# Performance work log

Hardware: AMD Instinct MI355X
Metric: run time of the kernel (lower is better)

Reference implementation:

```python
import jax, jax.numpy as jnp
import numpy as np

N, D, M, H, FF, L = 8192, 14, 36, 256, 2048, 2  # rows, d_model, material feats, mlp hidden, ffn, layers
EPS = 1e-5


def _ln(x, g, b):
    mu = jnp.mean(x, axis=-1, keepdims=True)
    var = jnp.mean((x - mu) ** 2, axis=-1, keepdims=True)
    return (x - mu) * jax.lax.rsqrt(var + EPS) * g + b


def setup_inputs() -> dict:
    key = jax.random.key(0)
    ks = iter(jax.random.split(key, 32))
    p = lambda shape, fan: jax.random.normal(next(ks), shape, jnp.float32) * (fan ** -0.5)
    return {
        "x": jax.random.normal(next(ks), (N, D), jnp.float32),
        "y": jax.random.normal(next(ks), (N, M), jnp.float32),
        # 2 post-LN TransformerEncoderLayers (nhead=1, dim_feedforward=2048, relu)
        "attn_wqkv": p((L, 3 * D, D), D), "attn_bqkv": p((L, 3 * D), D),
        "attn_wo": p((L, D, D), D), "attn_bo": p((L, D), D),
        "ln1_g": jnp.ones((L, D)), "ln1_b": jnp.zeros((L, D)),
        "ff_w1": p((L, FF, D), D), "ff_b1": p((L, FF), D),
        "ff_w2": p((L, D, FF), FF), "ff_b2": p((L, D), FF),
        "ln2_g": jnp.ones((L, D)), "ln2_b": jnp.zeros((L, D)),
        "fc1_w": p((D, D), D), "fc1_b": p((D,), D),
        "fc2_w": p((1, D), D), "fc2_b": p((1,), D),
        "fc3_w": p((H, D + M + 1), D + M + 1), "fc3_b": p((H,), D + M + 1),
        "fc4_w": p((H, H), H), "fc4_b": p((H,), H),
        "fc5_w": p((1, H), H), "fc5_b": p((1,), H),
    }


def reference(x, y, attn_wqkv, attn_bqkv, attn_wo, attn_bo, ln1_g, ln1_b,
              ff_w1, ff_b1, ff_w2, ff_b2, ln2_g, ln2_b,
              fc1_w, fc1_b, fc2_w, fc2_b, fc3_w, fc3_b, fc4_w, fc4_b, fc5_w, fc5_b):
    h = x  # [N, D]; batch of size 1 squeezed away
    for l in range(L):
        qkv = h @ attn_wqkv[l].T + attn_bqkv[l]            # [N, 3D]
        q, k, v = jnp.split(qkv, 3, axis=-1)
        scores = (q @ k.T) * (D ** -0.5)                   # [N, N]
        a = jax.nn.softmax(scores, axis=-1) @ v            # [N, D]
        a = a @ attn_wo[l].T + attn_bo[l]
        h = _ln(h + a, ln1_g[l], ln1_b[l])
        f = jax.nn.relu(h @ ff_w1[l].T + ff_b1[l]) @ ff_w2[l].T + ff_b2[l]
        h = _ln(h + f, ln2_g[l], ln2_b[l])
    x1 = h @ fc1_w.T + fc1_b                               # [N, D]
    size_out = (x1 @ fc2_w.T + fc2_b)[:, 0]                # [N]

    # batched replacement of the per-row python loop
    size_int = size_out.astype(jnp.int32)                  # trunc toward zero, like .int()
    size_f = size_int.astype(jnp.float32)[:, None]         # [N, 1]
    reg_in = jnp.concatenate([size_f, x, y], axis=1)       # [N, 1+D+M]
    r = jax.nn.relu(reg_in @ fc3_w.T + fc3_b)
    r = jax.nn.relu(r @ fc4_w.T + fc4_b)
    reg_values = (r @ fc5_w.T + fc5_b)[:, 0]               # [N]
    reg_values = jnp.where(size_int != 0, reg_values, 0.0)
    return size_out, reg_values
```

## Files before the change

kernel.cpp:

```cpp
#include <hip/hip_runtime.h>
#include <math.h>

#define NN 8192
#define DD 14
#define DP 16
#define FF 2048
#define HID 256
#define LN_EPS 1e-5f
#define QSCALE (1.4426950408889634f / 3.7416573867739413f)

typedef short bf16x8 __attribute__((ext_vector_type(8)));
typedef float f32x4 __attribute__((ext_vector_type(4)));

#define LOAD16(dst, srcp) { \
  const float4* _p = (const float4*)(srcp); \
  float4 _a = _p[0], _b = _p[1], _c = _p[2], _d = _p[3]; \
  dst[0]=_a.x; dst[1]=_a.y; dst[2]=_a.z; dst[3]=_a.w; \
  dst[4]=_b.x; dst[5]=_b.y; dst[6]=_b.z; dst[7]=_b.w; \
  dst[8]=_c.x; dst[9]=_c.y; dst[10]=_c.z; dst[11]=_c.w; \
  dst[12]=_d.x; dst[13]=_d.y; dst[14]=_d.z; dst[15]=_d.w; }

#define STORE16(dstp, src) { \
  float4* _p = (float4*)(dstp); \
  _p[0] = make_float4(src[0], src[1], src[2], src[3]); \
// ... 79 lines not shown
  VhiT[(size_t)15 * NN + r] = 0;
  VloT[(size_t)14 * NN + r] = 0;
  VloT[(size_t)15 * NN + r] = 0;
}

static __device__ __forceinline__ void store_apack(unsigned int* dst, const float* o) {
  unsigned int qp[16];
  unsigned short hh[14], ll[14];
  #pragma unroll
  for (int d = 0; d < 14; d++) {
    hh[d] = bf_hi(o[d]);
    ll[d] = bf_hi(o[d] - bf_hi_f(o[d]));
  }
  #pragma unroll
  for (int i = 0; i < 7; i++) {
    qp[i]     = (unsigned int)hh[2*i] | ((unsigned int)hh[2*i+1] << 16);
    qp[8 + i] = (unsigned int)ll[2*i] | ((unsigned int)ll[2*i+1] << 16);
  }
  qp[7] = 0; qp[15] = 0;
  uint4* d4 = (uint4*)dst;
  #pragma unroll
  for (int i = 0; i < 4; i++)
    d4[i] = make_uint4(qp[4*i], qp[4*i+1], qp[4*i+2], qp[4*i+3]);
}

static __device__ __forceinline__ void combine_ln1(
    const float* srow, const float* hr, const float* __restrict__ wo,
    const float* __restrict__ bo, const float* __restrict__ g,
    const float* __restrict__ b, float* o) {
  float L = srow[14];
  float inv = 1.f / L;
  float a[14];
  #pragma unroll
  for (int d = 0; d < 14; d++) a[d] = srow[d] * inv;
  float xx[14];
  #pragma unroll
  for (int i = 0; i < 14; i++) {
    float s = bo[i];
    #pragma unroll
    for (int d = 0; d < 14; d++) s = fmaf(wo[i * 14 + d], a[d], s);
    xx[i] = hr[i] + s;
  }
  float mu = 0.f;
  #pragma unroll
  for (int i = 0; i < 14; i++) mu += xx[i];
  mu *= (1.f / 14.f);
  float var = 0.f;
  #pragma unroll
  for (int i = 0; i < 14; i++) { float tt = xx[i] - mu; var = fmaf(tt, tt, var); }
  var *= (1.f / 14.f);
  float rs = rsqrtf(var + LN_EPS);
  #pragma unroll
  for (int i = 0; i < 14; i++) o[i] = fmaf((xx[i] - mu) * rs, g[i], b[i]);
  o[14] = 0.f; o[15] = 0.f;
}

__global__ void pack_all(const float* __restrict__ w3, const float* __restrict__ w4,
                         const float* __restrict__ ffw1, const float* __restrict__ ffw2,
                         const float* __restrict__ x, const float* __restrict__ wqkv,
                         const float* __restrict__ bqkv, float* __restrict__ h,
                         unsigned int* __restrict__ Qpack,
                         unsigned int* __restrict__ KB1, unsigned int* __restrict__ KB2,
                         unsigned short* __restrict__ VhiT, unsigned short* __restrict__ VloT,
                         unsigned short* __restrict__ B3h, unsigned short* __restrict__ B3l,
                         unsigned short* __restrict__ B4h, unsigned short* __restrict__ B4l,
                         unsigned int* __restrict__ W1B1, unsigned int* __restrict__ W1B2,
                         unsigned short* __restrict__ W2h, unsigned short* __restrict__ W2l) {
  const int blk = blockIdx.x, tid = threadIdx.x;
  if (blk < 32) {
    int t = blk * 256 + tid;
    int lane = t & 63, ks = (t >> 6) & 7, nt = t >> 9;
    int n = nt * 16 + (lane & 15);
    int k0 = ks * 32 + (lane >> 4) * 8;
    unsigned int h4[4], l4[4];
    #pragma unroll
    for (int jj = 0; jj < 4; jj++) {
      unsigned short h2[2], l2[2];
      #pragma unroll
      for (int e = 0; e < 2; e++) {
        float v = w4[(size_t)n * 256 + k0 + jj * 2 + e];
        h2[e] = bf_hi(v);
        l2[e] = bf_hi(v - bf_hi_f(v));
      }
      h4[jj] = (unsigned int)h2[0] | ((unsigned int)h2[1] << 16);
      l4[jj] = (unsigned int)l2[0] | ((unsigned int)l2[1] << 16);
    }
    ((uint4*)B4h)[t] = make_uint4(h4[0], h4[1], h4[2], h4[3]);
    ((uint4*)B4l)[t] = make_uint4(l4[0], l4[1], l4[2], l4[3]);
    if (ks < 2) {
      int fi = (nt * 2 + ks) * 64 + lane;
      #pragma unroll
      for (int jj = 0; jj < 4; jj++) {
        unsigned short h2[2], l2[2];
        #pragma unroll
        for (int e = 0; e < 2; e++) {
          int k = k0 + jj * 2 + e;
          float v = (k < 51) ? w3[(size_t)n * 51 + k] : 0.f;
          h2[e] = bf_hi(v);
          l2[e] = bf_hi(v - bf_hi_f(v));
        }
        h4[jj] = (unsigned int)h2[0] | ((unsigned int)h2[1] << 16);
        l4[jj] = (unsigned int)l2[0] | ((unsigned int)l2[1] << 16);
      }
      ((uint4*)B3h)[fi] = make_uint4(h4[0], h4[1], h4[2], h4[3]);
      ((uint4*)B3l)[fi] = make_uint4(l4[0], l4[1], l4[2], l4[3]);
    }
  } else if (blk < 48) {
    int t = (blk - 32) * 256 + tid;
    int l = t >> 11, j = t & 2047;
    const float* wrow = ffw1 + ((size_t)l * FF + j) * 14;
    unsigned int k1[16], k2[16];
    unsigned short kh[14], kl[14];
    #pragma unroll
    for (int d = 0; d < 14; d++) {
      float v = wrow[d];
      kh[d] = bf_hi(v);
      kl[d] = bf_hi(v - bf_hi_f(v));
    }
    #pragma unroll
    for (int i = 0; i < 7; i++) {
      k1[i] = (unsigned int)kh[2*i] | ((unsigned int)kh[2*i+1] << 16);
      k1[8 + i] = k1[i];
      k2[i] = (unsigned int)kl[2*i] | ((unsigned int)kl[2*i+1] << 16);
      k2[8 + i] = k2[i];
    }
    k1[7] = 0; k1[15] = 0; k2[7] = 0; k2[15] = 0;
    uint4* d1 = (uint4*)(W1B1 + (size_t)t * 16);
    uint4* d2 = (uint4*)(W1B2 + (size_t)t * 16);
    #pragma unroll
    for (int i = 0; i < 4; i++) {
      d1[i] = make_uint4(k1[4*i], k1[4*i+1], k1[4*i+2], k1[4*i+3]);
      d2[i] = make_uint4(k2[4*i], k2[4*i+1], k2[4*i+2], k2[4*i+3]);
    }
  } else if (blk < 64) {
    int t = (blk - 48) * 256 + tid;
    int l = t >> 11, j = t & 2047;
    #pragma unroll
    for (int d = 0; d < 16; d++) {
      float v = (d < 14) ? ffw2[((size_t)l * 14 + d) * FF + j] : 0.f;
      W2h[((size_t)l * 16 + d) * FF + j] = bf_hi(v);
      W2l[((size_t)l * 16 + d) * FF + j] = bf_hi(v - bf_hi_f(v));
    }
  } else {
    int r = (blk - 64) * 256 + tid;
    float hr[16];
    #pragma unroll
    for (int d = 0; d < 14; d++) hr[d] = x[(size_t)r * 14 + d];
    hr[14] = 0.f; hr[15] = 0.f;
    STORE16(h + (size_t)r * DP, hr);
    qkv_compute_store(r, hr, wqkv, bqkv, Qpack, KB1, KB2, VhiT, VloT);
  }
}

static __device__ __forceinline__ void attn_core(
    const bf16x8* __restrict__ Qp, const bf16x8* __restrict__ B1,
    const bf16x8* __restrict__ B2, const bf16x8* __restrict__ Vh,
    const bf16x8* __restrict__ Vl, int qbase, int wave, int lo4, int hi4,
    float (*Pl)[36], f32x4* o0, f32x4* o1) {
  const f32x4 zero = {0.f, 0.f, 0.f, 0.f};
  bf16x8 aQ0 = Qp[(size_t)(qbase + lo4) * 4 + hi4];
  bf16x8 aQ1 = Qp[(size_t)(qbase + 16 + lo4) * 4 + hi4];
  f32x4 acc0 = zero, acc1 = zero;
  const int kstart = wave * 1024;
  float4 ra0, ra1, rc0, rc1;
  const float4* p0 = (const float4*)&Pl[lo4][hi4 * 8];
  const float4* p1 = (const float4*)&Pl[16 + lo4][hi4 * 8];

  for (int c = 0; c < 32; c++) {
    const int kb = kstart + c * 32;
    if (c > 0) {
      ra0 = p0[0]; ra1 = p0[1]; rc0 = p1[0]; rc1 = p1[1];
      __asm__ volatile("" ::: "memory");
    }
    bf16x8 b1g0 = B1[(size_t)(kb + lo4) * 4 + hi4];
    bf16x8 b2g0 = B2[(size_t)(kb + lo4) * 4 + hi4];
    bf16x8 b1g1 = B1[(size_t)(kb + 16 + lo4) * 4 + hi4];
    bf16x8 b2g1 = B2[(size_t)(kb + 16 + lo4) * 4 + hi4];
    bf16x8 vh = Vh[(size_t)lo4 * 1024 + (kb >> 3) + hi4];
    bf16x8 vl = Vl[(size_t)lo4 * 1024 + (kb >> 3) + hi4];

    f32x4 s00 = __builtin_amdgcn_mfma_f32_16x16x32_bf16(aQ0, b1g0, zero, 0, 0, 0);
    f32x4 s01 = __builtin_amdgcn_mfma_f32_16x16x32_bf16(aQ0, b1g1, zero, 0, 0, 0);
    f32x4 s10 = __builtin_amdgcn_mfma_f32_16x16x32_bf16(aQ1, b1g0, zero, 0, 0, 0);
    f32x4 s11 = __builtin_amdgcn_mfma_f32_16x16x32_bf16(aQ1, b1g1, zero, 0, 0, 0);
    s00 = __builtin_amdgcn_mfma_f32_16x16x32_bf16(aQ0, b2g0, s00, 0, 0, 0);
    s01 = __builtin_amdgcn_mfma_f32_16x16x32_bf16(aQ0, b2g1, s01, 0, 0, 0);
    s10 = __builtin_amdgcn_mfma_f32_16x16x32_bf16(aQ1, b2g0, s10, 0, 0, 0);
    s11 = __builtin_amdgcn_mfma_f32_16x16x32_bf16(aQ1, b2g1, s11, 0, 0, 0);
    #pragma unroll
    for (int reg = 0; reg < 4; reg++) {
      Pl[hi4 * 4 + reg][lo4]           = fast_exp2(s00[reg]);
      Pl[hi4 * 4 + reg][16 + lo4]      = fast_exp2(s01[reg]);
      Pl[16 + hi4 * 4 + reg][lo4]      = fast_exp2(s10[reg]);
      Pl[16 + hi4 * 4 + reg][16 + lo4] = fast_exp2(s11[reg]);
    }
    if (c > 0) {
      const int kbp = kb - 32;
      bf16x8 vhp = Vh[(size_t)lo4 * 1024 + (kbp >> 3) + hi4];
      bf16x8 vlp = Vl[(size_t)lo4 * 1024 + (kbp >> 3) + hi4];
      float pv0[8] = {ra0.x, ra0.y, ra0.z, ra0.w, ra1.x, ra1.y, ra1.z, ra1.w};
      float pv1[8] = {rc0.x, rc0.y, rc0.z, rc0.w, rc1.x, rc1.y, rc1.z, rc1.w};
      bf16x8 ph0, pl0, ph1, pl1;
      split8(pv0, &ph0, &pl0);
      split8(pv1, &ph1, &pl1);
      acc0 = __builtin_amdgcn_mfma_f32_16x16x32_bf16(ph0, vhp, acc0, 0, 0, 0);
      acc1 = __builtin_amdgcn_mfma_f32_16x16x32_bf16(ph1, vhp, acc1, 0, 0, 0);
      acc0 = __builtin_amdgcn_mfma_f32_16x16x32_bf16(pl0, vhp, acc0, 0, 0, 0);
      acc1 = __builtin_amdgcn_mfma_f32_16x16x32_bf16(pl1, vhp, acc1, 0, 0, 0);
      acc0 = __builtin_amdgcn_mfma_f32_16x16x32_bf16(ph0, vlp, acc0, 0, 0, 0);
      acc1 = __builtin_amdgcn_mfma_f32_16x16x32_bf16(ph1, vlp, acc1, 0, 0, 0);
    }
  }
  {
    const int kbp = kstart + 31 * 32;
    bf16x8 vhp = Vh[(size_t)lo4 * 1024 + (kbp >> 3) + hi4];
    bf16x8 vlp = Vl[(size_t)lo4 * 1024 + (kbp >> 3) + hi4];
    float4 a0 = p0[0], a1 = p0[1], c0 = p1[0], c1 = p1[1];
    float pv0[8] = {a0.x, a0.y, a0.z, a0.w, a1.x, a1.y, a1.z, a1.w};
    float pv1[8] = {c0.x, c0.y, c0.z, c0.w, c1.x, c1.y, c1.z, c1.w};
    bf16x8 ph0, pl0, ph1, pl1;
    split8(pv0, &ph0, &pl0);
    split8(pv1, &ph1, &pl1);
    acc0 = __builtin_amdgcn_mfma_f32_16x16x32_bf16(ph0, vhp, acc0, 0, 0, 0);
    acc1 = __builtin_amdgcn_mfma_f32_16x16x32_bf16(ph1, vhp, acc1, 0, 0, 0);
    acc0 = __builtin_amdgcn_mfma_f32_16x16x32_bf16(pl0, vhp, acc0, 0, 0, 0);
    acc1 = __builtin_amdgcn_mfma_f32_16x16x32_bf16(pl1, vhp, acc1, 0, 0, 0);
    acc0 = __builtin_amdgcn_mfma_f32_16x16x32_bf16(ph0, vlp, acc0, 0, 0, 0);
    acc1 = __builtin_amdgcn_mfma_f32_16x16x32_bf16(ph1, vlp, acc1, 0, 0, 0);
  }
  *o0 = acc0; *o1 = acc1;
}

static __device__ __forceinline__ void ffn_core(
    bf16x8 aH0, bf16x8 aH1, const bf16x8* __restrict__ B1,
    const bf16x8* __restrict__ B2, const bf16x8* __restrict__ Vh,
    const bf16x8* __restrict__ Vl, const float* __restrict__ b1,
    int jstart, int lo4, int hi4, float (*Pl)[36], f32x4* o0, f32x4* o1) {
  const f32x4 zero = {0.f, 0.f, 0.f, 0.f};
  f32x4 acc0 = zero, acc1 = zero;
  float4 ra0, ra1, rc0, rc1;
  const float4* p0 = (const float4*)&Pl[lo4][hi4 * 8];
  const float4* p1 = (const float4*)&Pl[16 + lo4][hi4 * 8];

  for (int c = 0; c < 8; c++) {
    const int jb = jstart + c * 32;
    if (c > 0) {
      ra0 = p0[0]; ra1 = p0[1]; rc0 = p1[0]; rc1 = p1[1];
      __asm__ volatile("" ::: "memory");
    }
    bf16x8 b1g0 = B1[(size_t)(jb + lo4) * 4 + hi4];
    bf16x8 b2g0 = B2[(size_t)(jb + lo4) * 4 + hi4];
    bf16x8 b1g1 = B1[(size_t)(jb + 16 + lo4) * 4 + hi4];
    bf16x8 b2g1 = B2[(size_t)(jb + 16 + lo4) * 4 + hi4];
    float bb0 = b1[jb + lo4];
    float bb1 = b1[jb + 16 + lo4];

    f32x4 s00 = __builtin_amdgcn_mfma_f32_16x16x32_bf16(aH0, b1g0, zero, 0, 0, 0);
    f32x4 s01 = __builtin_amdgcn_mfma_f32_16x16x32_bf16(aH0, b1g1, zero, 0, 0, 0);
    f32x4 s10 = __builtin_amdgcn_mfma_f32_16x16x32_bf16(aH1, b1g0, zero, 0, 0, 0);
    f32x4 s11 = __builtin_amdgcn_mfma_f32_16x16x32_bf16(aH1, b1g1, zero, 0, 0, 0);
    s00 = __builtin_amdgcn_mfma_f32_16x16x32_bf16(aH0, b2g0, s00, 0, 0, 0);
    s01 = __builtin_amdgcn_mfma_f32_16x16x32_bf16(aH0, b2g1, s01, 0, 0, 0);
    s10 = __builtin_amdgcn_mfma_f32_16x16x32_bf16(aH1, b2g0, s10, 0, 0, 0);
    s11 = __builtin_amdgcn_mfma_f32_16x16x32_bf16(aH1, b2g1, s11, 0, 0, 0);
    #pragma unroll
    for (int reg = 0; reg < 4; reg++) {
      Pl[hi4 * 4 + reg][lo4]           = fmaxf(s00[reg] + bb0, 0.f);
      Pl[hi4 * 4 + reg][16 + lo4]      = fmaxf(s01[reg] + bb1, 0.f);
      Pl[16 + hi4 * 4 + reg][lo4]      = fmaxf(s10[reg] + bb0, 0.f);
      Pl[16 + hi4 * 4 + reg][16 + lo4] = fmaxf(s11[reg] + bb1, 0.f);
    }
    if (c > 0) {
      const int jbp = jb - 32;
      bf16x8 vhp = Vh[(size_t)lo4 * 256 + (jbp >> 3) + hi4];
      bf16x8 vlp = Vl[(size_t)lo4 * 256 + (jbp >> 3) + hi4];
      float pv0[8] = {ra0.x, ra0.y, ra0.z, ra0.w, ra1.x, ra1.y, ra1.z, ra1.w};
      float pv1[8] = {rc0.x, rc0.y, rc0.z, rc0.w, rc1.x, rc1.y, rc1.z, rc1.w};
      bf16x8 th0, tl0, th1, tl1;
      split8(pv0, &th0, &tl0);
      split8(pv1, &th1, &tl1);
      acc0 = __builtin_amdgcn_mfma_f32_16x16x32_bf16(th0, vhp, acc0, 0, 0, 0);
      acc1 = __builtin_amdgcn_mfma_f32_16x16x32_bf16(th1, vhp, acc1, 0, 0, 0);
      acc0 = __builtin_amdgcn_mfma_f32_16x16x32_bf16(tl0, vhp, acc0, 0, 0, 0);
      acc1 = __builtin_amdgcn_mfma_f32_16x16x32_bf16(tl1, vhp, acc1, 0, 0, 0);
      acc0 = __builtin_amdgcn_mfma_f32_16x16x32_bf16(th0, vlp, acc0, 0, 0, 0);
      acc1 = __builtin_amdgcn_mfma_f32_16x16x32_bf16(th1, vlp, acc1, 0, 0, 0);
    }
  }
  {
    const int jbp = jstart + 7 * 32;
    bf16x8 vhp = Vh[(size_t)lo4 * 256 + (jbp >> 3) + hi4];
    bf16x8 vlp = Vl[(size_t)lo4 * 256 + (jbp >> 3) + hi4];
    float4 a0 = p0[0], a1 = p0[1], c0 = p1[0], c1 = p1[1];
    float pv0[8] = {a0.x, a0.y, a0.z, a0.w, a1.x, a1.y, a1.z, a1.w};
    float pv1[8] = {c0.x, c0.y, c0.z, c0.w, c1.x, c1.y, c1.z, c1.w};
    bf16x8 th0, tl0, th1, tl1;
    split8(pv0, &th0, &tl0);
    split8(pv1, &th1, &tl1);
    acc0 = __builtin_amdgcn_mfma_f32_16x16x32_bf16(th0, vhp, acc0, 0, 0, 0);
    acc1 = __builtin_amdgcn_mfma_f32_16x16x32_bf16(th1, vhp, acc1, 0, 0, 0);
    acc0 = __builtin_amdgcn_mfma_f32_16x16x32_bf16(tl0, vhp, acc0, 0, 0, 0);
    acc1 = __builtin_amdgcn_mfma_f32_16x16x32_bf16(tl1, vhp, acc1, 0, 0, 0);
    acc0 = __builtin_amdgcn_mfma_f32_16x16x32_bf16(th0, vlp, acc0, 0, 0, 0);
    acc1 = __builtin_amdgcn_mfma_f32_16x16x32_bf16(th1, vlp, acc1, 0, 0, 0);
  }
  *o0 = acc0; *o1 = acc1;
}

#define SMEM_BYTES 57472

__global__ __launch_bounds__(512, 4) void layer0_fused(
    const unsigned int* __restrict__ Qpack, const unsigned int* __restrict__ KB1,
    const unsigned int* __restrict__ KB2, const unsigned short* __restrict__ VhiT,
    const unsigned short* __restrict__ VloT, float* __restrict__ h,
    const float* __restrict__ wo, const float* __restrict__ bo,
    const float* __restrict__ g1, const float* __restrict__ b1n,
    const unsigned int* __restrict__ W1B1, const unsigned int* __restrict__ W1B2,
    const unsigned short* __restrict__ W2h, const unsigned short* __restrict__ W2l,
    const float* __restrict__ fb1, const float* __restrict__ fb2,
    const float* __restrict__ g2, const float* __restrict__ b2n,
    const float* __restrict__ wqkv1, const float* __restrict__ bqkv1,
    unsigned int* __restrict__ Qpack1, unsigned int* __restrict__ KB1_1,
    unsigned int* __restrict__ KB2_1, unsigned short* __restrict__ VhiT1,
    unsigned short* __restrict__ VloT1) {
  __shared__ alignas(16) char smem[SMEM_BYTES];
  const int tid = threadIdx.x;
  const int wave = tid >> 6;
  const int lane = tid & 63;
  const int lo4 = lane & 15;
  const int hi4 = lane >> 4;
  const int qbase = blockIdx.x * 32;

  float (*Pl)[36] = (float(*)[36])(smem + wave * 4608);
  float (*sacc)[32][16] = (float(*)[32][16])(smem + 36864);
  float (*hrow)[16] = (float(*)[16])(smem + 53248);
  unsigned int (*Hl)[16] = (unsigned int(*)[16])(smem + 55296);

  f32x4 a0, a1;
  attn_core((const bf16x8*)Qpack, (const bf16x8*)KB1, (const bf16x8*)KB2,
            (const bf16x8*)VhiT, (const bf16x8*)VloT, qbase, wave, lo4, hi4,
            Pl, &a0, &a1);
  #pragma unroll
  for (int reg = 0; reg < 4; reg++) {
    sacc[wave][hi4 * 4 + reg][lo4] = a0[reg];
    sacc[wave][16 + hi4 * 4 + reg][lo4] = a1[reg];
  }
  __syncthreads();
  {
    int qq = tid >> 4, col = tid & 15;
    float v = 0.f;
    #pragma unroll
    for (int w = 0; w < 8; w++) v += sacc[w][qq][col];
    sacc[0][qq][col] = v;
  }
  __syncthreads();
  if (tid < 32) {
    int r = qbase + tid;
    float hr[16];
    LOAD16(hr, h + (size_t)r * DP);
    float o[16];
    combine_ln1(&sacc[0][tid][0], hr, wo, bo, g1, b1n, o);
    #pragma unroll
    for (int i = 0; i < 16; i++) hrow[tid][i] = o[i];
    store_apack(&Hl[tid][0], o);
  }
  __syncthreads();

  bf16x8 aH0 = *(const bf16x8*)&Hl[lo4][hi4 * 4];
  bf16x8 aH1 = *(const bf16x8*)&Hl[16 + lo4][hi4 * 4];
  f32x4 f0, f1;
  ffn_core(aH0, aH1, (const bf16x8*)W1B1, (const bf16x8*)W1B2,
           (const bf16x8*)W2h, (const bf16x8*)W2l, fb1, wave * 256,
           lo4, hi4, Pl, &f0, &f1);
  __syncthreads();
  #pragma unroll
  for (int reg = 0; reg < 4; reg++) {
    sacc[wave][hi4 * 4 + reg][lo4] = f0[reg];
    sacc[wave][16 + hi4 * 4 + reg][lo4] = f1[reg];
  }
  __syncthreads();
  {
    int qq = tid >> 4, col = tid & 15;
    float v = 0.f;
    #pragma unroll
    for (int w = 0; w < 8; w++) v += sacc[w][qq][col];
    sacc[0][qq][col] = v;
  }
  __syncthreads();
  if (tid < 32) {
    int r = qbase + tid;
    float xx[14];
    #pragma unroll
    for (int i = 0; i < 14; i++) xx[i] = hrow[tid][i] + sacc[0][tid][i] + fb2[i];
    float mu = 0.f;
    #pragma unroll
    for (int i = 0; i < 14; i++) mu += xx[i];
    mu *= (1.f / 14.f);
    float var = 0.f;
    #pragma unroll
    for (int i = 0; i < 14; i++) { float tt = xx[i] - mu; var = fmaf(tt, tt, var); }
    var *= (1.f / 14.f);
    float rs = rsqrtf(var + LN_EPS);
    float o[16];
    #pragma unroll
    for (int i = 0; i < 14; i++) o[i] = fmaf((xx[i] - mu) * rs, g2[i], b2n[i]);
    o[14] = 0.f; o[15] = 0.f;
    STORE16(h + (size_t)r * DP, o);
    qkv_compute_store(r, o, wqkv1, bqkv1, Qpack1, KB1_1, KB2_1, VhiT1, VloT1);
  }
}

__global__ __launch_bounds__(512, 4) void layer1_tail(
    const unsigned int* __restrict__ Qpack, const unsigned int* __restrict__ KB1,
    const unsigned int* __restrict__ KB2, const unsigned short* __restrict__ VhiT,
    const unsigned short* __restrict__ VloT, const float* __restrict__ h,
    const float* __restrict__ wo, const float* __restrict__ bo,
    const float* __restrict__ g1, const float* __restrict__ b1n,
    const unsigned int* __restrict__ W1B1, const unsigned int* __restrict__ W1B2,
    const unsigned short* __restrict__ W2h, const unsigned short* __restrict__ W2l,
    const float* __restrict__ fb1, const float* __restrict__ fb2,
    const float* __restrict__ g2, const float* __restrict__ b2n,
    const float* __restrict__ fc1w, const float* __restrict__ fc1b,
    const float* __restrict__ fc2w, const float* __restrict__ fc2b,
    const float* __restrict__ x, const float* __restrict__ y,
    const unsigned short* __restrict__ B3h, const unsigned short* __restrict__ B3l,
    const float* __restrict__ b3,
    const unsigned short* __restrict__ B4h, const unsigned short* __restrict__ B4l,
    const float* __restrict__ b4,
    const float* __restrict__ w5, const float* __restrict__ b5,
    float* __restrict__ out, float* __restrict__ outr) {
  __shared__ alignas(16) char smem[SMEM_BYTES];
  const int tid = threadIdx.x;
  const int wave = tid >> 6;
  const int lane = tid & 63;
  const int lo4 = lane & 15;
  const int hi4 = lane >> 4;
  const int qbase = blockIdx.x * 32;
  const f32x4 zero = {0.f, 0.f, 0.f, 0.f};

  float (*Pl)[36] = (float(*)[36])(smem + wave * 4608);
  float (*sacc)[32][16] = (float(*)[32][16])(smem + 36864);
  float (*hrow)[16] = (float(*)[16])(smem + 53248);
  unsigned int (*Hl)[16] = (unsigned int(*)[16])(smem + 55296);
  float* szf = (float*)(smem + 57344);

  f32x4 a0, a1;
  attn_core((const bf16x8*)Qpack, (const bf16x8*)KB1, (const bf16x8*)KB2,
            (const bf16x8*)VhiT, (const bf16x8*)VloT, qbase, wave, lo4, hi4,
            Pl, &a0, &a1);
  #pragma unroll
  for (int reg = 0; reg < 4; reg++) {
    sacc[wave][hi4 * 4 + reg][lo4] = a0[reg];
    sacc[wave][16 + hi4 * 4 + reg][lo4] = a1[reg];
  }
  __syncthreads();
  {
    int qq = tid >> 4, col = tid & 15;
    float v = 0.f;
    #pragma unroll
    for (int w = 0; w < 8; w++) v += sacc[w][qq][col];
    sacc[0][qq][col] = v;
  }
  __syncthreads();
  if (tid < 32) {
    int r = qbase + tid;
    float hr[16];
    LOAD16(hr, h + (size_t)r * DP);
    float o[16];
    combine_ln1(&sacc[0][tid][0], hr, wo, bo, g1, b1n, o);
    #pragma unroll
    for (int i = 0; i < 16; i++) hrow[tid][i] = o[i];
    store_apack(&Hl[tid][0], o);
  }
  __syncthreads();

  bf16x8 aH0 = *(const bf16x8*)&Hl[lo4][hi4 * 4];
  bf16x8 aH1 = *(const bf16x8*)&Hl[16 + lo4][hi4 * 4];
  f32x4 f0, f1;
  ffn_core(aH0, aH1, (const bf16x8*)W1B1, (const bf16x8*)W1B2,
           (const bf16x8*)W2h, (const bf16x8*)W2l, fb1, wave * 256,
           lo4, hi4, Pl, &f0, &f1);
  __syncthreads();
  #pragma unroll
  for (int reg = 0; reg < 4; reg++) {
    sacc[wave][hi4 * 4 + reg][lo4] = f0[reg];
    sacc[wave][16 + hi4 * 4 + reg][lo4] = f1[reg];
  }
  __syncthreads();
  {
    int qq = tid >> 4, col = tid & 15;
    float v = 0.f;
    #pragma unroll
    for (int w = 0; w < 8; w++) v += sacc[w][qq][col];
    sacc[0][qq][col] = v;
  }
  __syncthreads();
  if (tid < 32) {
    int r = qbase + tid;
    float xx[14];
    #pragma unroll
    for (int i = 0; i < 14; i++) xx[i] = hrow[tid][i] + sacc[0][tid][i] + fb2[i];
    float mu = 0.f;
    #pragma unroll
    for (int i = 0; i < 14; i++) mu += xx[i];
    mu *= (1.f / 14.f);
    float var = 0.f;
    #pragma unroll
    for (int i = 0; i < 14; i++) { float tt = xx[i] - mu; var = fmaf(tt, tt, var); }
    var *= (1.f / 14.f);
    float rs = rsqrtf(var + LN_EPS);
    float o[14];
    #pragma unroll
    for (int i = 0; i < 14; i++) o[i] = fmaf((xx[i] - mu) * rs, g2[i], b2n[i]);
    float s = fc2b[0];
    #pragma unroll
    for (int i = 0; i < 14; i++) {
      float tt = fc1b[i];
      #pragma unroll
      for (int d = 0; d < 14; d++) tt = fmaf(fc1w[i * 14 + d], o[d], tt);
      s = fmaf(tt, fc2w[i], s);
    }
    out[r] = s;
    int si = (int)s;
    szf[tid] = (float)si;
  }
  __syncthreads();

  const int grp = wave >> 2;
  const int wg  = wave & 3;

  for (int idx = tid; idx < 2 * 16 * 64; idx += 512) {
    int g = idx >> 10, m = (idx >> 6) & 15, k = idx & 63;
    int r = qbase + g * 16 + m;
    float v = 0.f;
    if (k == 0)       v = szf[g * 16 + m];
    else if (k < 15)  v = x[(size_t)r * 14 + (k - 1)];
    else if (k < 51)  v = y[(size_t)r * 36 + (k - 15)];
    ((unsigned short(*)[72])(smem + g * 2304))[m][k] = bf_hi(v);
    ((unsigned short(*)[72])(smem + 4608 + g * 2304))[m][k] = bf_hi(v - bf_hi_f(v));
  }
  __syncthreads();

  unsigned short (*Ah)[72]  = (unsigned short(*)[72])(smem + grp * 2304);
  unsigned short (*Al)[72]  = (unsigned short(*)[72])(smem + 4608 + grp * 2304);
  unsigned short (*R1h)[264] = (unsigned short(*)[264])(smem + 9216 + grp * 8448);
  unsigned short (*R1l)[264] = (unsigned short(*)[264])(smem + 26112 + grp * 8448);
  float (*sred)[16][16] = (float(*)[16][16])(smem + 43008 + (size_t)grp * 4096);

  f32x4 acc[4];
  #pragma unroll
  for (int nt = 0; nt < 4; nt++) acc[nt] = zero;
  #pragma unroll
  for (int ks = 0; ks < 2; ks++) {
    bf16x8 ah = *(const bf16x8*)&Ah[lo4][ks * 32 + hi4 * 8];
    bf16x8 al = *(const bf16x8*)&Al[lo4][ks * 32 + hi4 * 8];
    #pragma unroll
    for (int nt = 0; nt < 4; nt++) {
      int fi = ((wg * 4 + nt) * 2 + ks) * 64 + lane;
      bf16x8 bh = ((const bf16x8*)B3h)[fi];
      bf16x8 bl = ((const bf16x8*)B3l)[fi];
      acc[nt] = __builtin_amdgcn_mfma_f32_16x16x32_bf16(ah, bh, acc[nt], 0, 0, 0);
      acc[nt] = __builtin_amdgcn_mfma_f32_16x16x32_bf16(al, bh, acc[nt], 0, 0, 0);
      acc[nt] = __builtin_amdgcn_mfma_f32_16x16x32_bf16(ah, bl, acc[nt], 0, 0, 0);
    }
  }
  #pragma unroll
  for (int nt = 0; nt < 4; nt++) {
    int n = (wg * 4 + nt) * 16 + lo4;
    float bbv = b3[n];
    #pragma unroll
    for (int reg = 0; reg < 4; reg++) {
      int m = hi4 * 4 + reg;
      float v = fmaxf(acc[nt][reg] + bbv, 0.f);
      R1h[m][n] = bf_hi(v);
      R1l[m][n] = bf_hi(v - bf_hi_f(v));
    }
  }
  __syncthreads();

  #pragma unroll
  for (int nt = 0; nt < 4; nt++) acc[nt] = zero;
  #pragma unroll
  for (int ks = 0; ks < 8; ks++) {
    bf16x8 ah = *(const bf16x8*)&R1h[lo4][ks * 32 + hi4 * 8];
    bf16x8 al = *(const bf16x8*)&R1l[lo4][ks * 32 + hi4 * 8];
    #pragma unroll
    for (int nt = 0; nt < 4; nt++) {
      int fi = ((wg * 4 + nt) * 8 + ks) * 64 + lane;
      bf16x8 bh = ((const bf16x8*)B4h)[fi];
      bf16x8 bl = ((const bf16x8*)B4l)[fi];
      acc[nt] = __builtin_amdgcn_mfma_f32_16x16x32_bf16(ah, bh, acc[nt], 0, 0, 0);
      acc[nt] = __builtin_amdgcn_mfma_f32_16x16x32_bf16(al, bh, acc[nt], 0, 0, 0);
      acc[nt] = __builtin_amdgcn_mfma_f32_16x16x32_bf16(ah, bl, acc[nt], 0, 0, 0);
    }
  }
  float s4[4] = {0.f, 0.f, 0.f, 0.f};
  #pragma unroll
  for (int nt = 0; nt < 4; nt++) {
    int n = (wg * 4 + nt) * 16 + lo4;
    float bbv = b4[n], ww = w5[n];
    #pragma unroll
    for (int reg = 0; reg < 4; reg++)
      s4[reg] = fmaf(fmaxf(acc[nt][reg] + bbv, 0.f), ww, s4[reg]);
  }
  #pragma unroll
  for (int reg = 0; reg < 4; reg++) sred[wg][hi4 * 4 + reg][lo4] = s4[reg];
  __syncthreads();

  if (tid < 32) {
    int g = tid >> 4, m = tid & 15;
    float (*sredG)[16][16] = (float(*)[16][16])(smem + 43008 + (size_t)g * 4096);
    float t = b5[0];
    #pragma unroll
    for (int w = 0; w < 4; w++) {
      const float4* p = (const float4*)&sredG[w][m][0];
      float4 q0 = p[0], q1 = p[1], q2 = p[2], q3 = p[3];
      t += ((q0.x + q0.y) + (q0.z + q0.w)) + ((q1.x + q1.y) + (q1.z + q1.w)) +
           ((q2.x + q2.y) + (q2.z + q2.w)) + ((q3.x + q3.y) + (q3.z + q3.w));
    }
    float sz = szf[tid];
    outr[qbase + tid] = (sz != 0.f) ? t : 0.f;
  }
}

extern "C" void kernel_launch(void* const* d_in, const int* in_sizes, int n_in,
                              void* d_out, int out_size, void* d_ws, size_t ws_size,
                              hipStream_t stream) {
  const float* x    = (const float*)d_in[0];
  const float* y    = (const float*)d_in[1];
  const float* wqkv = (const float*)d_in[2];
  const float* bqkv = (const float*)d_in[3];
  const float* wo   = (const float*)d_in[4];
  const float* bo   = (const float*)d_in[5];
  const float* ln1g = (const float*)d_in[6];
  const float* ln1b = (const float*)d_in[7];
  const float* ffw1 = (const float*)d_in[8];
  const float* ffb1 = (const float*)d_in[9];
  const float* ffw2 = (const float*)d_in[10];
  const float* ffb2 = (const float*)d_in[11];
  const float* ln2g = (const float*)d_in[12];
  const float* ln2b = (const float*)d_in[13];
  const float* fc1w = (const float*)d_in[14];
  const float* fc1b = (const float*)d_in[15];
  const float* fc2w = (const float*)d_in[16];
  const float* fc2b = (const float*)d_in[17];
  const float* fc3w = (const float*)d_in[18];
  const float* fc3b = (const float*)d_in[19];
  const float* fc4w = (const float*)d_in[20];
  const float* fc4b = (const float*)d_in[21];
  const float* fc5w = (const float*)d_in[22];
  const float* fc5b = (const float*)d_in[23];

  float* ws = (float*)d_ws;
  float*          h      = ws;
  unsigned int*   Qpack0 = (unsigned int*)(ws + 131072);
  unsigned int*   KB1_0  = (unsigned int*)(ws + 262144);
  unsigned int*   KB2_0  = (unsigned int*)(ws + 393216);
  unsigned short* VhiT0  = (unsigned short*)(ws + 524288);
  unsigned short* VloT0  = (unsigned short*)(ws + 589824);
  unsigned int*   Qpack1 = (unsigned int*)(ws + 786432);
  unsigned int*   KB1_1  = (unsigned int*)(ws + 917504);
  unsigned int*   KB2_1  = (unsigned int*)(ws + 1048576);
  unsigned short* VhiT1  = (unsigned short*)(ws + 1179648);
  unsigned short* VloT1  = (unsigned short*)(ws + 1245184);
  unsigned short* B3h    = (unsigned short*)(ws + 2891776);
  unsigned short* B3l    = (unsigned short*)(ws + 2899968);
  unsigned short* B4h    = (unsigned short*)(ws + 2908160);
  unsigned short* B4l    = (unsigned short*)(ws + 2940928);
  unsigned int*   W1B1   = (unsigned int*)(ws + 2973696);
  unsigned int*   W1B2   = (unsigned int*)(ws + 3039232);
  unsigned short* W2h    = (unsigned short*)(ws + 3104768);
  unsigned short* W2l    = (unsigned short*)(ws + 3137536);

  float* out = (float*)d_out;

  pack_all<<<96, 256, 0, stream>>>(fc3w, fc4w, ffw1, ffw2, x, wqkv, bqkv, h,
                                   Qpack0, KB1_0, KB2_0, VhiT0, VloT0,
                                   B3h, B3l, B4h, B4l, W1B1, W1B2, W2h, W2l);

  layer0_fused<<<256, 512, 0, stream>>>(
      Qpack0, KB1_0, KB2_0, VhiT0, VloT0, h,
      wo, bo, ln1g, ln1b,
      W1B1, W1B2, W2h, W2l, ffb1, ffb2, ln2g, ln2b,
      wqkv + 42 * 14, bqkv + 42,
      Qpack1, KB1_1, KB2_1, VhiT1, VloT1);

  layer1_tail<<<256, 512, 0, stream>>>(
      Qpack1, KB1_1, KB2_1, VhiT1, VloT1, h,
      wo + 196, bo + 14, ln1g + 14, ln1b + 14,
      W1B1 + (size_t)2048 * 16, W1B2 + (size_t)2048 * 16,
      W2h + (size_t)16 * FF, W2l + (size_t)16 * FF,
      ffb1 + FF, ffb2 + 14, ln2g + 14, ln2b + 14,
      fc1w, fc1b, fc2w, fc2b, x, y,
      B3h, B3l, fc3b, B4h, B4l, fc4b,
      fc5w, fc5b, out, out + NN);
}
```

Baseline: 231.1 us.

## Halve query rows per block to 16 and double grid to 512 blocks

```diff
diff --git a/kernel.cpp b/kernel.cpp
--- a/kernel.cpp
+++ b/kernel.cpp
@@ -255,100 +255,79 @@
   }
 }
 
-static __device__ __forceinline__ void attn_core(
+static __device__ __forceinline__ void attn_core16(
     const bf16x8* __restrict__ Qp, const bf16x8* __restrict__ B1,
     const bf16x8* __restrict__ B2, const bf16x8* __restrict__ Vh,
     const bf16x8* __restrict__ Vl, int qbase, int wave, int lo4, int hi4,
-    float (*Pl)[36], f32x4* o0, f32x4* o1) {
+    float (*Pl)[36], f32x4* o0) {
   const f32x4 zero = {0.f, 0.f, 0.f, 0.f};
   bf16x8 aQ0 = Qp[(size_t)(qbase + lo4) * 4 + hi4];
-  bf16x8 aQ1 = Qp[(size_t)(qbase + 16 + lo4) * 4 + hi4];
-  f32x4 acc0 = zero, acc1 = zero;
+  f32x4 acc0 = zero;
   const int kstart = wave * 1024;
-  float4 ra0, ra1, rc0, rc1;
+  float4 ra0, ra1;
   const float4* p0 = (const float4*)&Pl[lo4][hi4 * 8];
-  const float4* p1 = (const float4*)&Pl[16 + lo4][hi4 * 8];
 
   for (int c = 0; c < 32; c++) {
     const int kb = kstart + c * 32;
     if (c > 0) {
-      ra0 = p0[0]; ra1 = p0[1]; rc0 = p1[0]; rc1 = p1[1];
+      ra0 = p0[0]; ra1 = p0[1];
       __asm__ volatile("" ::: "memory");
     }
     bf16x8 b1g0 = B1[(size_t)(kb + lo4) * 4 + hi4];
     bf16x8 b2g0 = B2[(size_t)(kb + lo4) * 4 + hi4];
     bf16x8 b1g1 = B1[(size_t)(kb + 16 + lo4) * 4 + hi4];
     bf16x8 b2g1 = B2[(size_t)(kb + 16 + lo4) * 4 + hi4];
-    bf16x8 vh = Vh[(size_t)lo4 * 1024 + (kb >> 3) + hi4];
-    bf16x8 vl = Vl[(size_t)lo4 * 1024 + (kb >> 3) + hi4];
 
     f32x4 s00 = __builtin_amdgcn_mfma_f32_16x16x32_bf16(aQ0, b1g0, zero, 0, 0, 0);
     f32x4 s01 = __builtin_amdgcn_mfma_f32_16x16x32_bf16(aQ0, b1g1, zero, 0, 0, 0);
-    f32x4 s10 = __builtin_amdgcn_mfma_f32_16x16x32_bf16(aQ1, b1g0, zero, 0, 0, 0);
-    f32x4 s11 = __builtin_amdgcn_mfma_f32_16x16x32_bf16(aQ1, b1g1, zero, 0, 0, 0);
     s00 = __builtin_amdgcn_mfma_f32_16x16x32_bf16(aQ0, b2g0, s00, 0, 0, 0);
     s01 = __builtin_amdgcn_mfma_f32_16x16x32_bf16(aQ0, b2g1, s01, 0, 0, 0);
-    s10 = __builtin_amdgcn_mfma_f32_16x16x32_bf16(aQ1, b2g0, s10, 0, 0, 0);
-    s11 = __builtin_amdgcn_mfma_f32_16x16x32_bf16(aQ1, b2g1, s11, 0, 0, 0);
     #pragma unroll
     for (int reg = 0; reg < 4; reg++) {
-      Pl[hi4 * 4 + reg][lo4]           = fast_exp2(s00[reg]);
-      Pl[hi4 * 4 + reg][16 + lo4]      = fast_exp2(s01[reg]);
-      Pl[16 + hi4 * 4 + reg][lo4]      = fast_exp2(s10[reg]);
-      Pl[16 + hi4 * 4 + reg][16 + lo4] = fast_exp2(s11[reg]);
+      Pl[hi4 * 4 + reg][lo4]      = fast_exp2(s00[reg]);
+      Pl[hi4 * 4 + reg][16 + lo4] = fast_exp2(s01[reg]);
     }
     if (c > 0) {
       const int kbp = kb - 32;
       bf16x8 vhp = Vh[(size_t)lo4 * 1024 + (kbp >> 3) + hi4];
       bf16x8 vlp = Vl[(size_t)lo4 * 1024 + (kbp >> 3) + hi4];
       float pv0[8] = {ra0.x, ra0.y, ra0.z, ra0.w, ra1.x, ra1.y, ra1.z, ra1.w};
-      float pv1[8] = {rc0.x, rc0.y, rc0.z, rc0.w, rc1.x, rc1.y, rc1.z, rc1.w};
-      bf16x8 ph0, pl0, ph1, pl1;
+      bf16x8 ph0, pl0;
       split8(pv0, &ph0, &pl0);
-      split8(pv1, &ph1, &pl1);
       acc0 = __builtin_amdgcn_mfma_f32_16x16x32_bf16(ph0, vhp, acc0, 0, 0, 0);
-      acc1 = __builtin_amdgcn_mfma_f32_16x16x32_bf16(ph1, vhp, acc1, 0, 0, 0);
       acc0 = __builtin_amdgcn_mfma_f32_16x16x32_bf16(pl0, vhp, acc0, 0, 0, 0);
-      acc1 = __builtin_amdgcn_mfma_f32_16x16x32_bf16(pl1, vhp, acc1, 0, 0, 0);
       acc0 = __builtin_amdgcn_mfma_f32_16x16x32_bf16(ph0, vlp, acc0, 0, 0, 0);
-      acc1 = __builtin_amdgcn_mfma_f32_16x16x32_bf16(ph1, vlp, acc1, 0, 0, 0);
     }
   }
   {
     const int kbp = kstart + 31 * 32;
     bf16x8 vhp = Vh[(size_t)lo4 * 1024 + (kbp >> 3) + hi4];
     bf16x8 vlp = Vl[(size_t)lo4 * 1024 + (kbp >> 3) + hi4];
-    float4 a0 = p0[0], a1 = p0[1], c0 = p1[0], c1 = p1[1];
+    float4 a0 = p0[0], a1 = p0[1];
     float pv0[8] = {a0.x, a0.y, a0.z, a0.w, a1.x, a1.y, a1.z, a1.w};
-    float pv1[8] = {c0.x, c0.y, c0.z, c0.w, c1.x, c1.y, c1.z, c1.w};
-    bf16x8 ph0, pl0, ph1, pl1;
+    bf16x8 ph0, pl0;
     split8(pv0, &ph0, &pl0);
-    split8(pv1, &ph1, &pl1);
     acc0 = __builtin_amdgcn_mfma_f32_16x16x32_bf16(ph0, vhp, acc0, 0, 0, 0);
-    acc1 = __builtin_amdgcn_mfma_f32_16x16x32_bf16(ph1, vhp, acc1, 0, 0, 0);
     acc0 = __builtin_amdgcn_mfma_f32_16x16x32_bf16(pl0, vhp, acc0, 0, 0, 0);
-    acc1 = __builtin_amdgcn_mfma_f32_16x16x32_bf16(pl1, vhp, acc1, 0, 0, 0);
     acc0 = __builtin_amdgcn_mfma_f32_16x16x32_bf16(ph0, vlp, acc0, 0, 0, 0);
-    acc1 = __builtin_amdgcn_mfma_f32_16x16x32_bf16(ph1, vlp, acc1, 0, 0, 0);
-  }
-  *o0 = acc0; *o1 = acc1;
-}
-
-static __device__ __forceinline__ void ffn_core(
-    bf16x8 aH0, bf16x8 aH1, const bf16x8* __restrict__ B1,
-    const bf16x8* __restrict__ B2, const bf16x8* __restrict__ Vh,
-    const bf16x8* __restrict__ Vl, const float* __restrict__ b1,
-    int jstart, int lo4, int hi4, float (*Pl)[36], f32x4* o0, f32x4* o1) {
+  }
+  *o0 = acc0;
+}
+
+static __device__ __forceinline__ void ffn_core16(
+    bf16x8 aH0, const bf16x8* __restrict__ B1, const bf16x8* __restrict__ B2,
+    const bf16x8* __restrict__ Vh, const bf16x8* __restrict__ Vl,
+    const float* __restrict__ b1, int jstart, int lo4, int hi4,
+    float (*Pl)[36], f32x4* o0) {
   const f32x4 zero = {0.f, 0.f, 0.f, 0.f};
-  f32x4 acc0 = zero, acc1 = zero;
-  float4 ra0, ra1, rc0, rc1;
+  f32x4 acc0 = zero;
+  float4 ra0, ra1;
   const float4* p0 = (const float4*)&Pl[lo4][hi4 * 8];
-  const float4* p1 = (const float4*)&Pl[16 + lo4][hi4 * 8];
 
   for (int c = 0; c < 8; c++) {
     const int jb = jstart + c * 32;
     if (c > 0) {
-      ra0 = p0[0]; ra1 = p0[1]; rc0 = p1[0]; rc1 = p1[1];
+      ra0 = p0[0]; ra1 = p0[1];
       __asm__ volatile("" ::: "memory");
     }
     bf16x8 b1g0 = B1[(size_t)(jb + lo4) * 4 + hi4];
@@ -360,57 +339,41 @@
 
     f32x4 s00 = __builtin_amdgcn_mfma_f32_16x16x32_bf16(aH0, b1g0, zero, 0, 0, 0);
     f32x4 s01 = __builtin_amdgcn_mfma_f32_16x16x32_bf16(aH0, b1g1, zero, 0, 0, 0);
-    f32x4 s10 = __builtin_amdgcn_mfma_f32_16x16x32_bf16(aH1, b1g0, zero, 0, 0, 0);
-    f32x4 s11 = __builtin_amdgcn_mfma_f32_16x16x32_bf16(aH1, b1g1, zero, 0, 0, 0);
     s00 = __builtin_amdgcn_mfma_f32_16x16x32_bf16(aH0, b2g0, s00, 0, 0, 0);
     s01 = __builtin_amdgcn_mfma_f32_16x16x32_bf16(aH0, b2g1, s01, 0, 0, 0);
-    s10 = __builtin_amdgcn_mfma_f32_16x16x32_bf16(aH1, b2g0, s10, 0, 0, 0);
-    s11 = __builtin_amdgcn_mfma_f32_16x16x32_bf16(aH1, b2g1, s11, 0, 0, 0);
     #pragma unroll
     for (int reg = 0; reg < 4; reg++) {
-      Pl[hi4 * 4 + reg][lo4]           = fmaxf(s00[reg] + bb0, 0.f);
-      Pl[hi4 * 4 + reg][16 + lo4]      = fmaxf(s01[reg] + bb1, 0.f);
-      Pl[16 + hi4 * 4 + reg][lo4]      = fmaxf(s10[reg] + bb0, 0.f);
-      Pl[16 + hi4 * 4 + reg][16 + lo4] = fmaxf(s11[reg] + bb1, 0.f);
+      Pl[hi4 * 4 + reg][lo4]      = fmaxf(s00[reg] + bb0, 0.f);
+      Pl[hi4 * 4 + reg][16 + lo4] = fmaxf(s01[reg] + bb1, 0.f);
     }
     if (c > 0) {
       const int jbp = jb - 32;
       bf16x8 vhp = Vh[(size_t)lo4 * 256 + (jbp >> 3) + hi4];
       bf16x8 vlp = Vl[(size_t)lo4 * 256 + (jbp >> 3) + hi4];
       float pv0[8] = {ra0.x, ra0.y, ra0.z, ra0.w, ra1.x, ra1.y, ra1.z, ra1.w};
-      float pv1[8] = {rc0.x, rc0.y, rc0.z, rc0.w, rc1.x, rc1.y, rc1.z, rc1.w};
-      bf16x8 th0, tl0, th1, tl1;
+      bf16x8 th0, tl0;
       split8(pv0, &th0, &tl0);
-      split8(pv1, &th1, &tl1);
       acc0 = __builtin_amdgcn_mfma_f32_16x16x32_bf16(th0, vhp, acc0, 0, 0, 0);
-      acc1 = __builtin_amdgcn_mfma_f32_16x16x32_bf16(th1, vhp, acc1, 0, 0, 0);
       acc0 = __builtin_amdgcn_mfma_f32_16x16x32_bf16(tl0, vhp, acc0, 0, 0, 0);
-      acc1 = __builtin_amdgcn_mfma_f32_16x16x32_bf16(tl1, vhp, acc1, 0, 0, 0);
       acc0 = __builtin_amdgcn_mfma_f32_16x16x32_bf16(th0, vlp, acc0, 0, 0, 0);
-      acc1 = __builtin_amdgcn_mfma_f32_16x16x32_bf16(th1, vlp, acc1, 0, 0, 0);
     }
   }
   {
     const int jbp = jstart + 7 * 32;
     bf16x8 vhp = Vh[(size_t)lo4 * 256 + (jbp >> 3) + hi4];
     bf16x8 vlp = Vl[(size_t)lo4 * 256 + (jbp >> 3) + hi4];
-    float4 a0 = p0[0], a1 = p0[1], c0 = p1[0], c1 = p1[1];
+    float4 a0 = p0[0], a1 = p0[1];
     float pv0[8] = {a0.x, a0.y, a0.z, a0.w, a1.x, a1.y, a1.z, a1.w};
-    float pv1[8] = {c0.x, c0.y, c0.z, c0.w, c1.x, c1.y, c1.z, c1.w};
-    bf16x8 th0, tl0, th1, tl1;
+    bf16x8 th0, tl0;
     split8(pv0, &th0, &tl0);
-    split8(pv1, &th1, &tl1);
     acc0 = __builtin_amdgcn_mfma_f32_16x16x32_bf16(th0, vhp, acc0, 0, 0, 0);
-    acc1 = __builtin_amdgcn_mfma_f32_16x16x32_bf16(th1, vhp, acc1, 0, 0, 0);
     acc0 = __builtin_amdgcn_mfma_f32_16x16x32_bf16(tl0, vhp, acc0, 0, 0, 0);
-    acc1 = __builtin_amdgcn_mfma_f32_16x16x32_bf16(tl1, vhp, acc1, 0, 0, 0);
     acc0 = __builtin_amdgcn_mfma_f32_16x16x32_bf16(th0, vlp, acc0, 0, 0, 0);
-    acc1 = __builtin_amdgcn_mfma_f32_16x16x32_bf16(th1, vlp, acc1, 0, 0, 0);
-  }
-  *o0 = acc0; *o1 = acc1;
-}
-
-#define SMEM_BYTES 57472
+  }
+  *o0 = acc0;
+}
+
+#define SMEM_BYTES 29760
 
 __global__ __launch_bounds__(512, 4) void layer0_fused(
     const unsigned int* __restrict__ Qpack, const unsigned int* __restrict__ KB1,
@@ -432,24 +395,22 @@
   const int lane = tid & 63;
   const int lo4 = lane & 15;
   const int hi4 = lane >> 4;
-  const int qbase = blockIdx.x * 32;
-
-  float (*Pl)[36] = (float(*)[36])(smem + wave * 4608);
-  float (*sacc)[32][16] = (float(*)[32][16])(smem + 36864);
-  float (*hrow)[16] = (float(*)[16])(smem + 53248);
-  unsigned int (*Hl)[16] = (unsigned int(*)[16])(smem + 55296);
-
-  f32x4 a0, a1;
-  attn_core((const bf16x8*)Qpack, (const bf16x8*)KB1, (const bf16x8*)KB2,
-            (const bf16x8*)VhiT, (const bf16x8*)VloT, qbase, wave, lo4, hi4,
-            Pl, &a0, &a1);
-  #pragma unroll
-  for (int reg = 0; reg < 4; reg++) {
+  const int qbase = blockIdx.x * 16;
+
+  float (*Pl)[36] = (float(*)[36])(smem + wave * 2304);
+  float (*sacc)[16][16] = (float(*)[16][16])(smem + 18432);
+  float (*hrow)[16] = (float(*)[16])(smem + 26624);
+  unsigned int (*Hl)[16] = (unsigned int(*)[16])(smem + 27648);
+
+  f32x4 a0;
+  attn_core16((const bf16x8*)Qpack, (const bf16x8*)KB1, (const bf16x8*)KB2,
+              (const bf16x8*)VhiT, (const bf16x8*)VloT, qbase, wave, lo4, hi4,
+              Pl, &a0);
+  #pragma unroll
+  for (int reg = 0; reg < 4; reg++)
     sacc[wave][hi4 * 4 + reg][lo4] = a0[reg];
-    sacc[wave][16 + hi4 * 4 + reg][lo4] = a1[reg];
-  }
-  __syncthreads();
-  {
+  __syncthreads();
+  if (tid < 256) {
     int qq = tid >> 4, col = tid & 15;
     float v = 0.f;
     #pragma unroll
@@ -457,7 +418,7 @@
     sacc[0][qq][col] = v;
   }
   __syncthreads();
-  if (tid < 32) {
+  if (tid < 16) {
     int r = qbase + tid;
     float hr[16];
     LOAD16(hr, h + (size_t)r * DP);
@@ -470,19 +431,15 @@
   __syncthreads();
 
   bf16x8 aH0 = *(const bf16x8*)&Hl[lo4][hi4 * 4];
-  bf16x8 aH1 = *(const bf16x8*)&Hl[16 + lo4][hi4 * 4];
-  f32x4 f0, f1;
-  ffn_core(aH0, aH1, (const bf16x8*)W1B1, (const bf16x8*)W1B2,
-           (const bf16x8*)W2h, (const bf16x8*)W2l, fb1, wave * 256,
-           lo4, hi4, Pl, &f0, &f1);
-  __syncthreads();
-  #pragma unroll
-  for (int reg = 0; reg < 4; reg++) {
+  f32x4 f0;
+  ffn_core16(aH0, (const bf16x8*)W1B1, (const bf16x8*)W1B2,
+             (const bf16x8*)W2h, (const bf16x8*)W2l, fb1, wave * 256,
+             lo4, hi4, Pl, &f0);
+  #pragma unroll
+  for (int reg = 0; reg < 4; reg++)
     sacc[wave][hi4 * 4 + reg][lo4] = f0[reg];
-    sacc[wave][16 + hi4 * 4 + reg][lo4] = f1[reg];
-  }
-  __syncthreads();
-  {
+  __syncthreads();
+  if (tid < 256) {
     int qq = tid >> 4, col = tid & 15;
     float v = 0.f;
     #pragma unroll
@@ -490,7 +447,7 @@
     sacc[0][qq][col] = v;
   }
   __syncthreads();
-  if (tid < 32) {
+  if (tid < 16) {
     int r = qbase + tid;
     float xx[14];
     #pragma unroll
@@ -538,26 +495,24 @@
   const int lane = tid & 63;
   const int lo4 = lane & 15;
   const int hi4 = lane >> 4;
-  const int qbase = blockIdx.x * 32;
+  const int qbase = blockIdx.x * 16;
   const f32x4 zero = {0.f, 0.f, 0.f, 0.f};
 
-  float (*Pl)[36] = (float(*)[36])(smem + wave * 4608);
-  float (*sacc)[32][16] = (float(*)[32][16])(smem + 36864);
-  float (*hrow)[16] = (float(*)[16])(smem + 53248);
-  unsigned int (*Hl)[16] = (unsigned int(*)[16])(smem + 55296);
-  float* szf = (float*)(smem + 57344);
-
-  f32x4 a0, a1;
-  attn_core((const bf16x8*)Qpack, (const bf16x8*)KB1, (const bf16x8*)KB2,
-            (const bf16x8*)VhiT, (const bf16x8*)VloT, qbase, wave, lo4, hi4,
-            Pl, &a0, &a1);
-  #pragma unroll
-  for (int reg = 0; reg < 4; reg++) {
+  float (*Pl)[36] = (float(*)[36])(smem + wave * 2304);
+  float (*sacc)[16][16] = (float(*)[16][16])(smem + 18432);
+  float (*hrow)[16] = (float(*)[16])(smem + 26624);
+  unsigned int (*Hl)[16] = (unsigned int(*)[16])(smem + 27648);
+  float* szf = (float*)(smem + 29696);
+
+  f32x4 a0;
+  attn_core16((const bf16x8*)Qpack, (const bf16x8*)KB1, (const bf16x8*)KB2,
+              (const bf16x8*)VhiT, (const bf16x8*)VloT, qbase, wave, lo4, hi4,
+              Pl, &a0);
+  #pragma unroll
+  for (int reg = 0; reg < 4; reg++)
     sacc[wave][hi4 * 4 + reg][lo4] = a0[reg];
-    sacc[wave][16 + hi4 * 4 + reg][lo4] = a1[reg];
-  }
-  __syncthreads();
-  {
+  __syncthreads();
+  if (tid < 256) {
     int qq = tid >> 4, col = tid & 15;
     float v = 0.f;
     #pragma unroll
@@ -565,7 +520,7 @@
     sacc[0][qq][col] = v;
   }
   __syncthreads();
-  if (tid < 32) {
+  if (tid < 16) {
     int r = qbase + tid;
     float hr[16];
     LOAD16(hr, h + (size_t)r * DP);
@@ -578,19 +533,15 @@
   __syncthreads();
 
   bf16x8 aH0 = *(const bf16x8*)&Hl[lo4][hi4 * 4];
-  bf16x8 aH1 = *(const bf16x8*)&Hl[16 + lo4][hi4 * 4];
-  f32x4 f0, f1;
-  ffn_core(aH0, aH1, (const bf16x8*)W1B1, (const bf16x8*)W1B2,
-           (const bf16x8*)W2h, (const bf16x8*)W2l, fb1, wave * 256,
-           lo4, hi4, Pl, &f0, &f1);
-  __syncthreads();
-  #pragma unroll
-  for (int reg = 0; reg < 4; reg++) {
+  f32x4 f0;
+  ffn_core16(aH0, (const bf16x8*)W1B1, (const bf16x8*)W1B2,
+             (const bf16x8*)W2h, (const bf16x8*)W2l, fb1, wave * 256,
+             lo4, hi4, Pl, &f0);
+  #pragma unroll
+  for (int reg = 0; reg < 4; reg++)
     sacc[wave][hi4 * 4 + reg][lo4] = f0[reg];
-    sacc[wave][16 + hi4 * 4 + reg][lo4] = f1[reg];
-  }
-  __syncthreads();
-  {
+  __syncthreads();
+  if (tid < 256) {
     int qq = tid >> 4, col = tid & 15;
     float v = 0.f;
     #pragma unroll
@@ -598,7 +549,7 @@
     sacc[0][qq][col] = v;
   }
   __syncthreads();
-  if (tid < 32) {
+  if (tid < 16) {
     int r = qbase + tid;
     float xx[14];
     #pragma unroll
@@ -629,37 +580,34 @@
   }
   __syncthreads();
 
-  const int grp = wave >> 2;
-  const int wg  = wave & 3;
-
-  for (int idx = tid; idx < 2 * 16 * 64; idx += 512) {
-    int g = idx >> 10, m = (idx >> 6) & 15, k = idx & 63;
-    int r = qbase + g * 16 + m;
+  unsigned short (*Ah)[72]  = (unsigned short(*)[72])(smem);
+  unsigned short (*Al)[72]  = (unsigned short(*)[72])(smem + 2304);
+  unsigned short (*R1h)[264] = (unsigned short(*)[264])(smem + 4608);
+  unsigned short (*R1l)[264] = (unsigned short(*)[264])(smem + 13056);
+  float (*sred)[16][16] = (float(*)[16][16])(smem + 21504);
+
+  for (int idx = tid; idx < 16 * 64; idx += 512) {
+    int m = idx >> 6, k = idx & 63;
+    int r = qbase + m;
     float v = 0.f;
-    if (k == 0)       v = szf[g * 16 + m];
+    if (k == 0)       v = szf[m];
     else if (k < 15)  v = x[(size_t)r * 14 + (k - 1)];
     else if (k < 51)  v = y[(size_t)r * 36 + (k - 15)];
-    ((unsigned short(*)[72])(smem + g * 2304))[m][k] = bf_hi(v);
-    ((unsigned short(*)[72])(smem + 4608 + g * 2304))[m][k] = bf_hi(v - bf_hi_f(v));
-  }
-  __syncthreads();
-
-  unsigned short (*Ah)[72]  = (unsigned short(*)[72])(smem + grp * 2304);
-  unsigned short (*Al)[72]  = (unsigned short(*)[72])(smem + 4608 + grp * 2304);
-  unsigned short (*R1h)[264] = (unsigned short(*)[264])(smem + 9216 + grp * 8448);
-  unsigned short (*R1l)[264] = (unsigned short(*)[264])(smem + 26112 + grp * 8448);
-  float (*sred)[16][16] = (float(*)[16][16])(smem + 43008 + (size_t)grp * 4096);
-
-  f32x4 acc[4];
-  #pragma unroll
-  for (int nt = 0; nt < 4; nt++) acc[nt] = zero;
+    Ah[m][k] = bf_hi(v);
+    Al[m][k] = bf_hi(v - bf_hi_f(v));
+  }
+  __syncthreads();
+
+  f32x4 acc[2];
+  #pragma unroll
+  for (int nt = 0; nt < 2; nt++) acc[nt] = zero;
   #pragma unroll
   for (int ks = 0; ks < 2; ks++) {
     bf16x8 ah = *(const bf16x8*)&Ah[lo4][ks * 32 + hi4 * 8];
     bf16x8 al = *(const bf16x8*)&Al[lo4][ks * 32 + hi4 * 8];
     #pragma unroll
-    for (int nt = 0; nt < 4; nt++) {
-      int fi = ((wg * 4 + nt) * 2 + ks) * 64 + lane;
+    for (int nt = 0; nt < 2; nt++) {
+      int fi = ((wave * 2 + nt) * 2 + ks) * 64 + lane;
       bf16x8 bh = ((const bf16x8*)B3h)[fi];
       bf16x8 bl = ((const bf16x8*)B3l)[fi];
       acc[nt] = __builtin_amdgcn_mfma_f32_16x16x32_bf16(ah, bh, acc[nt], 0, 0, 0);
@@ -668,8 +616,8 @@
     }
   }
   #pragma unroll
-  for (int nt = 0; nt < 4; nt++) {
-    int n = (wg * 4 + nt) * 16 + lo4;
+  for (int nt = 0; nt < 2; nt++) {
+    int n = (wave * 2 + nt) * 16 + lo4;
     float bbv = b3[n];
     #pragma unroll
     for (int reg = 0; reg < 4; reg++) {
@@ -682,14 +630,14 @@
   __syncthreads();
 
   #pragma unroll
-  for (int nt = 0; nt < 4; nt++) acc[nt] = zero;
+  for (int nt = 0; nt < 2; nt++) acc[nt] = zero;
   #pragma unroll
   for (int ks = 0; ks < 8; ks++) {
     bf16x8 ah = *(const bf16x8*)&R1h[lo4][ks * 32 + hi4 * 8];
     bf16x8 al = *(const bf16x8*)&R1l[lo4][ks * 32 + hi4 * 8];
     #pragma unroll
-    for (int nt = 0; nt < 4; nt++) {
-      int fi = ((wg * 4 + nt) * 8 + ks) * 64 + lane;
+    for (int nt = 0; nt < 2; nt++) {
+      int fi = ((wave * 2 + nt) * 8 + ks) * 64 + lane;
       bf16x8 bh = ((const bf16x8*)B4h)[fi];
       bf16x8 bl = ((const bf16x8*)B4l)[fi];
       acc[nt] = __builtin_amdgcn_mfma_f32_16x16x32_bf16(ah, bh, acc[nt], 0, 0, 0);
@@ -699,24 +647,22 @@
   }
   float s4[4] = {0.f, 0.f, 0.f, 0.f};
   #pragma unroll
-  for (int nt = 0; nt < 4; nt++) {
-    int n = (wg * 4 + nt) * 16 + lo4;
+  for (int nt = 0; nt < 2; nt++) {
+    int n = (wave * 2 + nt) * 16 + lo4;
     float bbv = b4[n], ww = w5[n];
     #pragma unroll
     for (int reg = 0; reg < 4; reg++)
       s4[reg] = fmaf(fmaxf(acc[nt][reg] + bbv, 0.f), ww, s4[reg]);
   }
   #pragma unroll
-  for (int reg = 0; reg < 4; reg++) sred[wg][hi4 * 4 + reg][lo4] = s4[reg];
-  __syncthreads();
-
-  if (tid < 32) {
-    int g = tid >> 4, m = tid & 15;
-    float (*sredG)[16][16] = (float(*)[16][16])(smem + 43008 + (size_t)g * 4096);
+  for (int reg = 0; reg < 4; reg++) sred[wave][hi4 * 4 + reg][lo4] = s4[reg];
+  __syncthreads();
+
+  if (tid < 16) {
     float t = b5[0];
     #pragma unroll
-    for (int w = 0; w < 4; w++) {
-      const float4* p = (const float4*)&sredG[w][m][0];
+    for (int w = 0; w < 8; w++) {
+      const float4* p = (const float4*)&sred[w][tid][0];
       float4 q0 = p[0], q1 = p[1], q2 = p[2], q3 = p[3];
       t += ((q0.x + q0.y) + (q0.z + q0.w)) + ((q1.x + q1.y) + (q1.z + q1.w)) +
            ((q2.x + q2.y) + (q2.z + q2.w)) + ((q3.x + q3.y) + (q3.z + q3.w));
@@ -781,14 +727,14 @@
                                    Qpack0, KB1_0, KB2_0, VhiT0, VloT0,
                                    B3h, B3l, B4h, B4l, W1B1, W1B2, W2h, W2l);
 
-  layer0_fused<<<256, 512, 0, stream>>>(
+  layer0_fused<<<512, 512, 0, stream>>>(
       Qpack0, KB1_0, KB2_0, VhiT0, VloT0, h,
       wo, bo, ln1g, ln1b,
       W1B1, W1B2, W2h, W2l, ffb1, ffb2, ln2g, ln2b,
       wqkv + 42 * 14, bqkv + 42,
       Qpack1, KB1_1, KB2_1, VhiT1, VloT1);
 
-  layer1_tail<<<256, 512, 0, stream>>>(
+  layer1_tail<<<512, 512, 0, stream>>>(
       Qpack1, KB1_1, KB2_1, VhiT1, VloT1, h,
       wo + 196, bo + 14, ln1g + 14, ln1b + 14,
       W1B1 + (size_t)2048 * 16, W1B2 + (size_t)2048 * 16,
```

New measurement: 286.0 us. 1.24x slower.
